# Optimization experiments

Measured on AMD Instinct MI355X. Metric: run time of the kernel, lower is better.

The kernel has to match this reference:

```python
import jax, jax.numpy as jnp
import numpy as np

HIDDEN = 1024   # hidden_dimensions (dim_in)
NUM_HEADS = 16
HEAD_DIM = 64   # dim_q == dim_k == output_dimensions per head
BATCH = 4
SEQ = 2048


def setup_inputs() -> dict:
    key = jax.random.key(0)
    ks = jax.random.split(key, 11)
    s = 1.0 / np.sqrt(HIDDEN)
    so = 1.0 / np.sqrt(NUM_HEADS * HEAD_DIM)
    return {
        "Q": jax.random.normal(ks[0], (BATCH, SEQ, HIDDEN), jnp.float32),
        "K": jax.random.normal(ks[1], (BATCH, SEQ, HIDDEN), jnp.float32),
        "V": jax.random.normal(ks[2], (BATCH, SEQ, HIDDEN), jnp.float32),
        # per-head projection weights stacked over the head axis
        "Wq": jax.random.uniform(ks[3], (NUM_HEADS, HIDDEN, HEAD_DIM), jnp.float32, -s, s),
        "bq": jax.random.uniform(ks[4], (NUM_HEADS, HEAD_DIM), jnp.float32, -s, s),
        "Wk": jax.random.uniform(ks[5], (NUM_HEADS, HIDDEN, HEAD_DIM), jnp.float32, -s, s),
        "bk": jax.random.uniform(ks[6], (NUM_HEADS, HEAD_DIM), jnp.float32, -s, s),
        "Wv": jax.random.uniform(ks[7], (NUM_HEADS, HIDDEN, HEAD_DIM), jnp.float32, -s, s),
        "bv": jax.random.uniform(ks[8], (NUM_HEADS, HEAD_DIM), jnp.float32, -s, s),
        # output projection: concat(num_heads*head_dim) -> hidden
        "Wo": jax.random.uniform(ks[9], (NUM_HEADS * HEAD_DIM, HIDDEN), jnp.float32, -so, so),
        "bo": jax.random.uniform(ks[10], (HIDDEN,), jnp.float32, -so, so),
    }


def reference(Q, K, V, Wq, bq, Wk, bk, Wv, bv, Wo, bo):
    # Per-head linear projections (batched over heads instead of Python loop)
    q = jnp.einsum("bsd,hdk->bhsk", Q, Wq) + bq[None, :, None, :]  # [B,H,S,dk]
    k = jnp.einsum("bsd,hdk->bhsk", K, Wk) + bk[None, :, None, :]
    v = jnp.einsum("bsd,hdk->bhsk", V, Wv) + bv[None, :, None, :]
    # Scaled dot-product attention
    scale = 1.0 / jnp.sqrt(jnp.asarray(k.shape[-1], q.dtype))
    scores = jnp.einsum("bhqk,bhsk->bhqs", q, k) * scale          # [B,H,S,S]
    attn = jax.nn.softmax(scores, axis=-1)
    o = jnp.einsum("bhqs,bhsk->bhqk", attn, v)                     # [B,H,S,dk]
    # Concatenate heads along the feature dim, then output linear
    B, H, S, dk = o.shape
    concat = jnp.transpose(o, (0, 2, 1, 3)).reshape(B, S, H * dk)  # [B,S,H*dk]
    return concat @ Wo + bo                                        # [B,S,HIDDEN]
```

## Files before the change

kernel.cpp:

```cpp
#include <hip/hip_runtime.h>
#include <hip/hip_bf16.h>
#include <stdint.h>

typedef unsigned short u16;
typedef uint32_t u32;
typedef __attribute__((ext_vector_type(4))) float f32x4;
typedef __attribute__((ext_vector_type(16))) float f32x16;
typedef __attribute__((ext_vector_type(8))) short s8v;
typedef __attribute__((ext_vector_type(4))) unsigned short u16x4;
typedef __attribute__((ext_vector_type(2))) uint32_t u32x2;
typedef __attribute__((ext_vector_type(4))) uint32_t u32x4;

#define SCALE_Q 0.18033688f

union PU { s8v v; u32 w[4]; };

__device__ __forceinline__ u16 f2bf(float f) {
  union { float f; uint32_t u; } v; v.f = f;
  uint32_t r = v.u + 0x7fffu + ((v.u >> 16) & 1u);
  return (u16)(r >> 16);
}

__device__ __forceinline__ u32 pk2(float lo, float hi) {
  __hip_bfloat162 h = __float22bfloat162_rn(float2{lo, hi});
  union { __hip_bfloat162 h; u32 u; } c; c.h = h; return c.u;
}

__device__ __forceinline__ void gl16(const void* g, void* l) {
  __builtin_amdgcn_global_load_lds((const __attribute__((address_space(1))) u32*)g,
                                   (__attribute__((address_space(3))) u32*)l, 16, 0, 0);
}

#define BARRIER()  __builtin_amdgcn_s_barrier()
#define SCHEDB()   __builtin_amdgcn_sched_barrier(0)
#define SGB(m, n)  __builtin_amdgcn_sched_group_barrier((m), (n), 0)
#define MEMPIN()   asm volatile("" ::: "memory")

__global__ __launch_bounds__(256) void k_convW_t(const float* __restrict__ wq, const float* __restrict__ wk,
                                                 const float* __restrict__ wv, u16* __restrict__ oq,
                                                 u16* __restrict__ ok, u16* __restrict__ ov) {
  __shared__ float T[64][65];
  const int z = blockIdx.z, h = blockIdx.y, d0 = blockIdx.x * 64;
  const float* w = z == 0 ? wq : (z == 1 ? wk : wv);
  u16* o = z == 0 ? oq : (z == 1 ? ok : ov);
  const float scale = z == 0 ? SCALE_Q : 1.0f;
  const int t = threadIdx.x;
#pragma unroll
  for (int i = 0; i < 16; ++i) {
    int f = t + i * 256;
    T[f >> 6][f & 63] = w[(h * 1024 + d0 + (f >> 6)) * 64 + (f & 63)];
  }
  __syncthreads();
#pragma unroll
  for (int i = 0; i < 16; ++i) {
    int g = t + i * 256;
    o[(h * 64 + (g >> 6)) * 1024 + d0 + (g & 63)] = f2bf(T[g & 63][g >> 6] * scale);
  }
}

__global__ __launch_bounds__(256) void k_convWo_t(const float* __restrict__ w, u16* __restrict__ o) {
  __shared__ float T[64][65];
  const int n0 = blockIdx.x * 64, c0 = blockIdx.y * 64;
  const int t = threadIdx.x;
#pragma unroll
  for (int i = 0; i < 16; ++i) {
    int f = t + i * 256;
    T[f >> 6][f & 63] = w[(c0 + (f >> 6)) * 1024 + n0 + (f & 63)];
  }
  __syncthreads();
#pragma unroll
  for (int i = 0; i < 16; ++i) {
    int g = t + i * 256;
    o[(n0 + (g >> 6)) * 1024 + c0 + (g & 63)] = f2bf(T[g & 63][g >> 6]);
  }
}

__global__ __launch_bounds__(256) void k_gemm3f(
    const float* __restrict__ Aq, const float* __restrict__ Ak, const float* __restrict__ Av,
    const u16* __restrict__ Bq, const u16* __restrict__ Bk, const u16* __restrict__ Bv,
    const float* __restrict__ bqp, const float* __restrict__ bkp, const float* __restrict__ bvp,
    u16* __restrict__ oq, u16* __restrict__ ok, u16* __restrict__ ov) {
  constexpr int Kd = 1024, Nd = 1024;
  __shared__ alignas(16) u16 As[128 * 64];
  __shared__ alignas(16) u16 Bs[128 * 64];
  const int z = blockIdx.z;
  const float* A = z == 0 ? Aq : (z == 1 ? Ak : Av);
  const u16* Bt = z == 0 ? Bq : (z == 1 ? Bk : Bv);
  const float* bias = z == 0 ? bqp : (z == 1 ? bkp : bvp);

  const int t = threadIdx.x;
  const int lane = t & 63;
  const int w = t >> 6;
  const int wm = w >> 1, wn = w & 1;
  const int lr = lane & 15, lg = lane >> 4;
  const long bm = blockIdx.x * 128, bn = blockIdx.y * 128;
  const int r8 = lane >> 3, c8 = lane & 7;
  const int chunk = c8 ^ r8;

  const int arow_s = t >> 3, achk = t & 7;
  const int aswz = (achk ^ (arow_s & 7)) * 8;
  const float* Apf = A + (bm + arow_s) * (long)Kd + achk * 8;
  const u16* Bp = Bt + (bn + w * 8 + r8) * (long)Kd + chunk * 8;

  f32x4 acc[4][4] = {};
  float4 fa[4][2];

  auto ALOAD = [&](int kt) {
#pragma unroll
    for (int j = 0; j < 4; ++j) {
      fa[j][0] = *(const float4*)(Apf + (long)j * 32 * Kd + kt);
      fa[j][1] = *(const float4*)(Apf + (long)j * 32 * Kd + kt + 4);
    }
  };
  auto AWRITE = [&]() {
#pragma unroll
    for (int j = 0; j < 4; ++j) {
      u32x4 pk;
      pk[0] = pk2(fa[j][0].x, fa[j][0].y);
      pk[1] = pk2(fa[j][0].z, fa[j][0].w);
      pk[2] = pk2(fa[j][1].x, fa[j][1].y);
      pk[3] = pk2(fa[j][1].z, fa[j][1].w);
      *(u32x4*)(&As[(j * 32 + arow_s) * 64 + aswz]) = pk;
    }
  };
  auto BSTG = [&](int kt) {
#pragma unroll
    for (int p = 0; p < 4; ++p)
      gl16(Bp + (long)p * 32 * Kd + kt, Bs + (p * 32 + w * 8) * 64);
  };
  auto GCOMP = [&]() {
#pragma unroll
    for (int ks = 0; ks < 2; ++ks) {
      s8v af[4], bf[4];
#pragma unroll
      for (int i = 0; i < 4; ++i) {
        int arow = wm * 64 + i * 16 + lr;
        af[i] = *(const s8v*)(&As[arow * 64 + (((ks * 4 + lg) ^ (arow & 7)) * 8)]);
        int brow = wn * 64 + i * 16 + lr;
        bf[i] = *(const s8v*)(&Bs[brow * 64 + (((ks * 4 + lg) ^ (brow & 7)) * 8)]);
      }
#pragma unroll
      for (int i = 0; i < 4; ++i)
#pragma unroll
        for (int j = 0; j < 4; ++j)
          acc[i][j] = __builtin_amdgcn_mfma_f32_16x16x32_bf16(af[i], bf[j], acc[i][j], 0, 0, 0);
    }
  };

  ALOAD(0);
  for (int kt = 0; kt < 16; ++kt) {
    BARRIER();
    SCHEDB();
    AWRITE();
    MEMPIN();
    BSTG(kt * 64);
    MEMPIN();
    if (kt < 15) {
      ALOAD((kt + 1) * 64);
      MEMPIN();
      asm volatile("s_waitcnt vmcnt(8) lgkmcnt(0)" ::: "memory");
    } else {
      asm volatile("s_waitcnt vmcnt(0) lgkmcnt(0)" ::: "memory");
    }
    SCHEDB();
    BARRIER();
    SCHEDB();
    GCOMP();
  }

  const float bscale = z == 0 ? SCALE_Q : 1.0f;
  float bcol[4];
#pragma unroll
  for (int j = 0; j < 4; ++j) bcol[j] = bias[bn + wn * 64 + j * 16 + lr] * bscale;

  if (z < 2) {
    u16* C = z == 0 ? oq : ok;
#pragma unroll
    for (int i = 0; i < 4; ++i) {
      long m0 = bm + wm * 64 + i * 16 + lg * 4;
#pragma unroll
      for (int j = 0; j < 4; ++j) {
        long n = bn + wn * 64 + j * 16 + lr;
#pragma unroll
        for (int r = 0; r < 4; ++r)
          C[(m0 + r) * Nd + n] = f2bf(acc[i][j][r] + bcol[j]);
      }
    }
  } else {
    u16* C = ov;
    int lgp = ((lg & 1) << 1) | (lg >> 1);
#pragma unroll
    for (int i = 0; i < 4; ++i) {
      long m0 = bm + wm * 64 + i * 16 + lgp * 4;
      int b = (int)(m0 >> 11), s0 = (int)(m0 & 2047);
#pragma unroll
      for (int j = 0; j < 4; ++j) {
        int n = (int)(bn + wn * 64 + j * 16 + lr);
        int h = n >> 6, dv = n & 63;
        u32x2 cc;
        cc[0] = pk2(acc[i][j][0] + bcol[j], acc[i][j][1] + bcol[j]);
        cc[1] = pk2(acc[i][j][2] + bcol[j], acc[i][j][3] + bcol[j]);
        *(u32x2*)(C + (long)((b * 16 + h) * 64 + dv) * 2048 + s0) = cc;
      }
    }
  }
}

__global__ __launch_bounds__(256) void k_gemmo(const u16* __restrict__ A, const u16* __restrict__ Bt,
                                               const float* __restrict__ bias, float* __restrict__ C) {
  constexpr int Kd = 1024, Nd = 1024;
  __shared__ alignas(16) u16 As[2][128 * 64];
  __shared__ alignas(16) u16 Bs[2][128 * 64];
  const int t = threadIdx.x;
  const int lane = t & 63;
  const int w = t >> 6;
  const int wm = w >> 1, wn = w & 1;
  const int lr = lane & 15, lg = lane >> 4;
  const long bm = blockIdx.x * 128, bn = blockIdx.y * 128;
  const int r8 = lane >> 3, c8 = lane & 7;
  const int chunk = c8 ^ r8;

  f32x4 acc[4][4] = {};
  const u16* Ap = A + (bm + w * 8 + r8) * (long)Kd + chunk * 8;
  const u16* Bp = Bt + (bn + w * 8 + r8) * (long)Kd + chunk * 8;

  auto GSTAGE = [&](u16* Asb, u16* Bsb, int kt) {
#pragma unroll
    for (int p = 0; p < 4; ++p) {
      gl16(Ap + (long)p * 32 * Kd + kt, Asb + (p * 32 + w * 8) * 64);
      gl16(Bp + (long)p * 32 * Kd + kt, Bsb + (p * 32 + w * 8) * 64);
    }
  };
  auto GCOMP = [&](const u16* Asb, const u16* Bsb) {
#pragma unroll
    for (int ks = 0; ks < 2; ++ks) {
      s8v af[4], bf[4];
#pragma unroll
      for (int i = 0; i < 4; ++i) {
        int arow = wm * 64 + i * 16 + lr;
        af[i] = *(const s8v*)(Asb + arow * 64 + (((ks * 4 + lg) ^ (arow & 7)) * 8));
        int brow = wn * 64 + i * 16 + lr;
        bf[i] = *(const s8v*)(Bsb + brow * 64 + (((ks * 4 + lg) ^ (brow & 7)) * 8));
      }
#pragma unroll
      for (int i = 0; i < 4; ++i)
#pragma unroll
        for (int j = 0; j < 4; ++j)
          acc[i][j] = __builtin_amdgcn_mfma_f32_16x16x32_bf16(af[i], bf[j], acc[i][j], 0, 0, 0);
    }
  };

  GSTAGE(As[0], Bs[0], 0);
  for (int kt = 0; kt < 16; ++kt) {
    BARRIER();
    SCHEDB();
    if (kt < 15) {
      GSTAGE(As[(kt + 1) & 1], Bs[(kt + 1) & 1], (kt + 1) * 64);
      asm volatile("s_waitcnt vmcnt(8)" ::: "memory");
    } else {
      asm volatile("s_waitcnt vmcnt(0)" ::: "memory");
    }
    SCHEDB();
    BARRIER();
    SCHEDB();
    GCOMP(As[kt & 1], Bs[kt & 1]);
  }

  float bcol[4];
#pragma unroll
  for (int j = 0; j < 4; ++j) bcol[j] = bias[bn + wn * 64 + j * 16 + lr];
#pragma unroll
  for (int i = 0; i < 4; ++i) {
    long m0 = bm + wm * 64 + i * 16 + lg * 4;
#pragma unroll
    for (int j = 0; j < 4; ++j) {
      long n = bn + wn * 64 + j * 16 + lr;
#pragma unroll
      for (int r = 0; r < 4; ++r)
        C[(m0 + r) * Nd + n] = acc[i][j][r] + bcol[j];
    }
  }
}

__global__ __launch_bounds__(256, 2) void k_attn(const u16* __restrict__ q, const u16* __restrict__ k,
                                                 const u16* __restrict__ vT, u16* __restrict__ o) {
  __shared__ alignas(16) u16 Ks[4][64 * 64];
  __shared__ alignas(16) u16 Vs[4][64 * 64];
  const int t = threadIdx.x;
  const int lane = t & 63;
  const int wv = t >> 6;
  const int l5 = lane & 31, hi = lane >> 5;
  const int r8 = lane >> 3, c8 = lane & 7;
  const int rx = l5 & 7;

  const int wg = blockIdx.x;
  const int ob = (wg & 7) * 64 + (wg >> 3);
  const int qt = ob & 7, h = (ob >> 3) & 15, b = ob >> 7;

  const int qrow0 = qt * 256 + wv * 64 + l5;
  const u16* qpA = q + ((long)(b * 2048 + qrow0) * 1024 + h * 64);
  const u16* qpB = qpA + 32 * 1024;
  s8v qfA[4], qfB[4];
#pragma unroll
  for (int s = 0; s < 4; ++s) {
    qfA[s] = *(const s8v*)(qpA + s * 16 + hi * 8);
    qfB[s] = *(const s8v*)(qpB + s * 16 + hi * 8);
  }

  const u16* Kpp = k + (long)b * 2048 * 1024 + h * 64 + (long)r8 * 1024 + ((c8 ^ r8) * 8);
  const u16* Vpp = vT + (long)(b * 16 + h) * 131072 + (long)r8 * 2048 + ((c8 ^ r8) * 8);

  f32x16 accA0 = {}, accA1 = {}, accB0 = {}, accB1 = {};
  float lA = 0.f, lB = 0.f;

  int offs[4];
#pragma unroll
  for (int s = 0; s < 4; ++s) offs[s] = ((2 * s + hi) ^ rx) * 8;
  const int rb0 = l5 * 64, rb1 = rb0 + 2048;

  auto ASTAGE = [&](int buf, int kv) {
#pragma unroll
    for (int r0 = 0; r0 < 2; ++r0) {
      int rowo = wv * 16 + r0 * 8;
      gl16(Kpp + ((long)kv + rowo) * 1024, &Ks[buf][rowo * 64]);
      gl16(Vpp + (long)rowo * 2048 + kv,   &Vs[buf][rowo * 64]);
    }
  };

  auto EXPPACK = [&](const f32x16& sv, PU& u0, PU& u1, float& l) {
#pragma unroll
    for (int r1 = 0; r1 < 4; ++r1) {
      float p0 = __builtin_amdgcn_exp2f(sv[4 * r1 + 0]);
      float p1 = __builtin_amdgcn_exp2f(sv[4 * r1 + 1]);
      float p2 = __builtin_amdgcn_exp2f(sv[4 * r1 + 2]);
      float p3 = __builtin_amdgcn_exp2f(sv[4 * r1 + 3]);
      l += (p0 + p1) + (p2 + p3);
      if (r1 < 2) {
        u0.w[(r1 & 1) * 2 + 0] = pk2(p0, p1);
        u0.w[(r1 & 1) * 2 + 1] = pk2(p2, p3);
      } else {
        u1.w[(r1 & 1) * 2 + 0] = pk2(p0, p1);
        u1.w[(r1 & 1) * 2 + 1] = pk2(p2, p3);
      }
    }
  };

  auto ATILE = [&](int buf) {
    const u16* Ksb = Ks[buf];
    const u16* Vsb = Vs[buf];
    PU paU[4], pbU[4];
    f32x16 sA0 = {}, sB0 = {}, sA1 = {}, sB1 = {};
    s8v kf0[4], kf1[4];
#pragma unroll
    for (int s = 0; s < 4; ++s) {
      kf0[s] = *(const s8v*)(Ksb + rb0 + offs[s]);
      kf1[s] = *(const s8v*)(Ksb + rb1 + offs[s]);
    }
#pragma unroll
    for (int s = 0; s < 4; ++s) {
      sA0 = __builtin_amdgcn_mfma_f32_32x32x16_bf16(kf0[s], qfA[s], sA0, 0, 0, 0);
      sB0 = __builtin_amdgcn_mfma_f32_32x32x16_bf16(kf0[s], qfB[s], sB0, 0, 0, 0);
    }
#pragma unroll
    for (int g = 0; g < 4; ++g) { SGB(0x100, 2); SGB(0x8, 2); }
    SCHEDB();
#pragma unroll
    for (int s = 0; s < 4; ++s) {
      sA1 = __builtin_amdgcn_mfma_f32_32x32x16_bf16(kf1[s], qfA[s], sA1, 0, 0, 0);
      sB1 = __builtin_amdgcn_mfma_f32_32x32x16_bf16(kf1[s], qfB[s], sB1, 0, 0, 0);
    }
    EXPPACK(sA0, paU[0], paU[1], lA);
    EXPPACK(sB0, pbU[0], pbU[1], lB);
#pragma unroll
    for (int g = 0; g < 8; ++g) { SGB(0x8, 1); SGB(0x2, 9); }
    SCHEDB();
    s8v vf0[4], vf1[4];
#pragma unroll
    for (int s = 0; s < 4; ++s) {
      vf0[s] = *(const s8v*)(Vsb + rb0 + offs[s]);
      vf1[s] = *(const s8v*)(Vsb + rb1 + offs[s]);
    }
#pragma unroll
    for (int s2 = 0; s2 < 2; ++s2) {
      accA0 = __builtin_amdgcn_mfma_f32_32x32x16_bf16(vf0[s2], paU[s2].v, accA0, 0, 0, 0);
      accA1 = __builtin_amdgcn_mfma_f32_32x32x16_bf16(vf1[s2], paU[s2].v, accA1, 0, 0, 0);
      accB0 = __builtin_amdgcn_mfma_f32_32x32x16_bf16(vf0[s2], pbU[s2].v, accB0, 0, 0, 0);
      accB1 = __builtin_amdgcn_mfma_f32_32x32x16_bf16(vf1[s2], pbU[s2].v, accB1, 0, 0, 0);
    }
    EXPPACK(sA1, paU[2], paU[3], lA);
    EXPPACK(sB1, pbU[2], pbU[3], lB);
#pragma unroll
    for (int g = 0; g < 8; ++g) { SGB(0x100, 1); SGB(0x8, 1); SGB(0x2, 9); }
    SCHEDB();
#pragma unroll
    for (int s2 = 2; s2 < 4; ++s2) {
      accA0 = __builtin_amdgcn_mfma_f32_32x32x16_bf16(vf0[s2], paU[s2].v, accA0, 0, 0, 0);
      accA1 = __builtin_amdgcn_mfma_f32_32x32x16_bf16(vf1[s2], paU[s2].v, accA1, 0, 0, 0);
      accB0 = __builtin_amdgcn_mfma_f32_32x32x16_bf16(vf0[s2], pbU[s2].v, accB0, 0, 0, 0);
      accB1 = __builtin_amdgcn_mfma_f32_32x32x16_bf16(vf1[s2], pbU[s2].v, accB1, 0, 0, 0);
    }
  };

  ASTAGE(0, 0);
  ASTAGE(1, 64);
  asm volatile("s_waitcnt vmcnt(4)" ::: "memory");
  SCHEDB();
  BARRIER();
  SCHEDB();
  for (int tt = 0; tt < 30; ++tt) {
    ASTAGE((tt + 2) & 3, (tt + 2) * 64);
    ATILE(tt & 3);
    asm volatile("s_waitcnt vmcnt(4) lgkmcnt(0)" ::: "memory");
    SCHEDB();
    BARRIER();
    SCHEDB();
  }
  ATILE(30 & 3);
  asm volatile("s_waitcnt vmcnt(0) lgkmcnt(0)" ::: "memory");
  SCHEDB();
  BARRIER();
  SCHEDB();
  ATILE(31 & 3);

  lA += __shfl_xor(lA, 32);
  lB += __shfl_xor(lB, 32);
  float iA = 1.0f / lA, iB = 1.0f / lB;
  u16* opA = o + ((long)(b * 2048 + qrow0) * 1024 + h * 64);
  u16* opB = opA + 32 * 1024;
#pragma unroll
  for (int kb = 0; kb < 2; ++kb) {
#pragma unroll
    for (int r1 = 0; r1 < 4; ++r1) {
      u32x2 ca, cb;
      float a0 = kb ? accA1[4 * r1 + 0] : accA0[4 * r1 + 0];
      float a1 = kb ? accA1[4 * r1 + 1] : accA0[4 * r1 + 1];
      float a2 = kb ? accA1[4 * r1 + 2] : accA0[4 * r1 + 2];
      float a3 = kb ? accA1[4 * r1 + 3] : accA0[4 * r1 + 3];
      ca[0] = pk2(a0 * iA, a1 * iA);
      ca[1] = pk2(a2 * iA, a3 * iA);
      *(u32x2*)(opA + kb * 32 + r1 * 8 + hi * 4) = ca;
      float b0v = kb ? accB1[4 * r1 + 0] : accB0[4 * r1 + 0];
      float b1v = kb ? accB1[4 * r1 + 1] : accB0[4 * r1 + 1];
      float b2v = kb ? accB1[4 * r1 + 2] : accB0[4 * r1 + 2];
      float b3v = kb ? accB1[4 * r1 + 3] : accB0[4 * r1 + 3];
      cb[0] = pk2(b0v * iB, b1v * iB);
      cb[1] = pk2(b2v * iB, b3v * iB);
      *(u32x2*)(opB + kb * 32 + r1 * 8 + hi * 4) = cb;
    }
  }
}

extern "C" void kernel_launch(void* const* d_in, const int* in_sizes, int n_in,
                              void* d_out, int out_size, void* d_ws, size_t ws_size,
                              hipStream_t stream) {
  const float* Q  = (const float*)d_in[0];
  const float* K  = (const float*)d_in[1];
  const float* V  = (const float*)d_in[2];
  const float* Wq = (const float*)d_in[3];
  const float* bq = (const float*)d_in[4];
  const float* Wk = (const float*)d_in[5];
  const float* bk = (const float*)d_in[6];
  const float* Wv = (const float*)d_in[7];
  const float* bvp = (const float*)d_in[8];
  const float* Wo = (const float*)d_in[9];
  const float* bo = (const float*)d_in[10];
  float* out = (float*)d_out;

  char* ws = (char*)d_ws;
  const size_t MB16 = (size_t)8192 * 1024 * 2;
  u16* WqT = (u16*)(ws);
  u16* WkT = (u16*)(ws + ((size_t)2 << 20));
  u16* WvT = (u16*)(ws + ((size_t)4 << 20));
  u16* WoT = (u16*)(ws + ((size_t)6 << 20));
  u16* qws = (u16*)(ws + ((size_t)8 << 20));
  u16* kws = (u16*)(ws + ((size_t)8 << 20) + MB16);
  u16* vTs = (u16*)(ws + ((size_t)8 << 20) + 2 * MB16);
  u16* ows = (u16*)(ws + ((size_t)8 << 20) + 3 * MB16);

  k_convW_t<<<dim3(16, 16, 3), 256, 0, stream>>>(Wq, Wk, Wv, WqT, WkT, WvT);
  k_convWo_t<<<dim3(16, 16), 256, 0, stream>>>(Wo, WoT);

  k_gemm3f<<<dim3(64, 8, 3), 256, 0, stream>>>(Q, K, V, WqT, WkT, WvT,
                                               bq, bk, bvp, qws, kws, vTs);

  k_attn<<<dim3(512), 256, 0, stream>>>(qws, kws, vTs, ows);

  k_gemmo<<<dim3(64, 8), 256, 0, stream>>>(ows, WoT, bo, out);
}
```

Before: 186.2 us.

## Double-buffer shared memory tiles in the QKV projection GEMM

Splits the A and B shared-memory tiles of the fused QKV projection GEMM into two buffers. Each iteration now writes the next k-tile's converted A data and issues the next B direct-to-LDS loads into the spare buffer while computing on the current one, with global A loads running two steps ahead. The goal is to overlap staging and global-load latency with MFMA work and drop the vmcnt wait inside the loop. The cost is twice the LDS per block, which may lower occupancy, and correctness now depends on in-order completion of vector memory loads to make sure the B tile has landed.

```diff
diff --git a/kernel.cpp b/kernel.cpp
--- a/kernel.cpp
+++ b/kernel.cpp
@@ -81,8 +81,8 @@
     const float* __restrict__ bqp, const float* __restrict__ bkp, const float* __restrict__ bvp,
     u16* __restrict__ oq, u16* __restrict__ ok, u16* __restrict__ ov) {
   constexpr int Kd = 1024, Nd = 1024;
-  __shared__ alignas(16) u16 As[128 * 64];
-  __shared__ alignas(16) u16 Bs[128 * 64];
+  __shared__ alignas(16) u16 As[2][128 * 64];
+  __shared__ alignas(16) u16 Bs[2][128 * 64];
   const int z = blockIdx.z;
   const float* A = z == 0 ? Aq : (z == 1 ? Ak : Av);
   const u16* Bt = z == 0 ? Bq : (z == 1 ? Bk : Bv);
@@ -112,7 +112,7 @@
       fa[j][1] = *(const float4*)(Apf + (long)j * 32 * Kd + kt + 4);
     }
   };
-  auto AWRITE = [&]() {
+  auto AWRITE = [&](u16* Asb) {
 #pragma unroll
     for (int j = 0; j < 4; ++j) {
       u32x4 pk;
@@ -120,24 +120,24 @@
       pk[1] = pk2(fa[j][0].z, fa[j][0].w);
       pk[2] = pk2(fa[j][1].x, fa[j][1].y);
       pk[3] = pk2(fa[j][1].z, fa[j][1].w);
-      *(u32x4*)(&As[(j * 32 + arow_s) * 64 + aswz]) = pk;
-    }
-  };
-  auto BSTG = [&](int kt) {
+      *(u32x4*)(Asb + (j * 32 + arow_s) * 64 + aswz) = pk;
+    }
+  };
+  auto BSTG = [&](u16* Bsb, int kt) {
 #pragma unroll
     for (int p = 0; p < 4; ++p)
-      gl16(Bp + (long)p * 32 * Kd + kt, Bs + (p * 32 + w * 8) * 64);
-  };
-  auto GCOMP = [&]() {
+      gl16(Bp + (long)p * 32 * Kd + kt, Bsb + (p * 32 + w * 8) * 64);
+  };
+  auto GCOMP = [&](const u16* Asb, const u16* Bsb) {
 #pragma unroll
     for (int ks = 0; ks < 2; ++ks) {
       s8v af[4], bf[4];
 #pragma unroll
       for (int i = 0; i < 4; ++i) {
         int arow = wm * 64 + i * 16 + lr;
-        af[i] = *(const s8v*)(&As[arow * 64 + (((ks * 4 + lg) ^ (arow & 7)) * 8)]);
+        af[i] = *(const s8v*)(Asb + arow * 64 + (((ks * 4 + lg) ^ (arow & 7)) * 8));
         int brow = wn * 64 + i * 16 + lr;
-        bf[i] = *(const s8v*)(&Bs[brow * 64 + (((ks * 4 + lg) ^ (brow & 7)) * 8)]);
+        bf[i] = *(const s8v*)(Bsb + brow * 64 + (((ks * 4 + lg) ^ (brow & 7)) * 8));
       }
 #pragma unroll
       for (int i = 0; i < 4; ++i)
@@ -148,24 +148,30 @@
   };
 
   ALOAD(0);
+  AWRITE(As[0]);
+  MEMPIN();
+  BSTG(Bs[0], 0);
+  MEMPIN();
+  ALOAD(64);
+
   for (int kt = 0; kt < 16; ++kt) {
     BARRIER();
     SCHEDB();
-    AWRITE();
-    MEMPIN();
-    BSTG(kt * 64);
-    MEMPIN();
     if (kt < 15) {
-      ALOAD((kt + 1) * 64);
+      AWRITE(As[(kt + 1) & 1]);
       MEMPIN();
-      asm volatile("s_waitcnt vmcnt(8) lgkmcnt(0)" ::: "memory");
+      BSTG(Bs[(kt + 1) & 1], (kt + 1) * 64);
+      MEMPIN();
+      if (kt < 14) ALOAD((kt + 2) * 64);
+      MEMPIN();
+      asm volatile("s_waitcnt lgkmcnt(0)" ::: "memory");
     } else {
       asm volatile("s_waitcnt vmcnt(0) lgkmcnt(0)" ::: "memory");
     }
     SCHEDB();
     BARRIER();
     SCHEDB();
-    GCOMP();
+    GCOMP(As[kt & 1], Bs[kt & 1]);
   }
 
   const float bscale = z == 0 ? SCALE_Q : 1.0f;
```

Measured after the change: 196.5 us. 1.06x slower.
